# Optimization experiments

Hardware: AMD Instinct MI355X
Metric: run time of the kernel (lower is better)

## Reference

```python
import jax, jax.numpy as jnp
import numpy as np
from jax import lax

EPS = 1e-8
CAGE_SIZE = 1.4
DIST_THRESH = 0.4
CAGE_ITERS = 100
CAGE_STEP = 0.01


def _icosphere_div1():
    # icosahedron with one loop subdivision -> 42 verts, 80 faces, unit sphere
    t = (1.0 + 5.0 ** 0.5) / 2.0
    v = np.array([[-1, t, 0], [1, t, 0], [-1, -t, 0], [1, -t, 0],
                  [0, -1, t], [0, 1, t], [0, -1, -t], [0, 1, -t],
                  [t, 0, -1], [t, 0, 1], [-t, 0, -1], [-t, 0, 1]], dtype=np.float64)
    v /= np.linalg.norm(v, axis=1, keepdims=True)
    f = [[0, 11, 5], [0, 5, 1], [0, 1, 7], [0, 7, 10], [0, 10, 11],
         [1, 5, 9], [5, 11, 4], [11, 10, 2], [10, 7, 6], [7, 1, 8],
         [3, 9, 4], [3, 4, 2], [3, 2, 6], [3, 6, 8], [3, 8, 9],
         [4, 9, 5], [2, 4, 11], [6, 2, 10], [8, 6, 7], [9, 8, 1]]
    verts = list(v)
    cache = {}
    def mid(a, b):
        key = (min(a, b), max(a, b))
        if key not in cache:
            m = verts[a] + verts[b]
            verts.append(m / np.linalg.norm(m))
            cache[key] = len(verts) - 1
        return cache[key]
    nf = []
    for a, b, c in f:
        ab, bc, ca = mid(a, b), mid(b, c), mid(c, a)
        nf += [[a, ab, ca], [b, bc, ab], [c, ca, bc], [ab, bc, ca]]
    return np.stack(verts).astype(np.float32), np.array(nf, dtype=np.int32)


def _optimize_cage(cage, shape):
    # cage: (B,3,V), shape: (B,3,N). Pull cage toward origin until close to shape.
    def step(c, _):
        diff = c[:, :, :, None] - shape[:, :, None, :]          # (B,3,V,N)
        dist = jnp.sqrt(jnp.sum(diff * diff, axis=1))           # (B,V,N)
        min_d = jnp.min(dist, axis=2)                           # (B,V)
        upd = (min_d > DIST_THRESH).astype(c.dtype)
        return c + CAGE_STEP * (-c) * upd[:, None], None
    cage, _ = lax.scan(step, cage, None, length=CAGE_ITERS)
    return cage


def _mvc_weights(query, verts, faces):
    # 3D mean value coordinates (Ju et al. 2005).
    # query: (B,P,3), verts: (B,V,3), faces: (F,3) int -> weights (B,P,V)
    B, P, _ = query.shape
    V = verts.shape[1]
    F = faces.shape[0]
    u = verts[:, None] - query[:, :, None]                      # (B,P,V,3)
    d = jnp.linalg.norm(u, axis=-1)                             # (B,P,V)
    u = u / jnp.maximum(d, EPS)[..., None]
    uf = u[:, :, faces]                                         # (B,P,F,3,3)
    df = d[:, :, faces]                                         # (B,P,F,3)
    # edge lengths on unit sphere between opposite corner directions
    l = jnp.linalg.norm(jnp.roll(uf, -1, axis=3) - jnp.roll(uf, 1, axis=3), axis=-1)  # (B,P,F,3)
    theta = 2.0 * jnp.arcsin(jnp.clip(0.5 * l, 0.0, 1.0))
    h = 0.5 * jnp.sum(theta, axis=-1)                           # (B,P,F)
    sin_t = jnp.sin(theta)
    c = (2.0 * jnp.sin(h)[..., None] * jnp.sin(h[..., None] - theta)
         / jnp.maximum(jnp.roll(sin_t, -1, axis=-1) * jnp.roll(sin_t, 1, axis=-1), EPS)) - 1.0
    u0, u1, u2 = uf[..., 0, :], uf[..., 1, :], uf[..., 2, :]
    det = jnp.sum(u0 * jnp.cross(u1, u2), axis=-1)              # (B,P,F)
    s = jnp.sign(det)[..., None] * jnp.sqrt(jnp.clip(1.0 - c * c, 0.0, None))  # (B,P,F,3)
    valid = jnp.all(jnp.abs(s) > EPS, axis=-1)                  # coplanar-outside -> face contributes 0
    num = (theta - jnp.roll(c, -1, axis=-1) * jnp.roll(theta, 1, axis=-1)
           - jnp.roll(c, 1, axis=-1) * jnp.roll(theta, -1, axis=-1))
    den = df * jnp.roll(sin_t, -1, axis=-1) * jnp.roll(s, 1, axis=-1)
    den = jnp.where(jnp.abs(den) > EPS, den, jnp.where(den >= 0, EPS, -EPS))
    w = jnp.where(valid[..., None], num / den, 0.0)             # (B,P,F,3)
    W = jnp.zeros((B, P, V), dtype=query.dtype).at[:, :, faces.reshape(-1)].add(
        w.reshape(B, P, F * 3))
    sW = jnp.sum(W, axis=-1, keepdims=True)
    sW = jnp.where(jnp.abs(sW) > EPS, sW, EPS)
    return W / sW


def setup_inputs() -> dict:
    key = jax.random.key(0)
    ks = jax.random.split(key, 5)
    B, N, K = 4, 6144, 8
    v, f = _icosphere_div1()
    template_vertices = jnp.asarray(CAGE_SIZE * v.T[None])      # (1,3,42)
    return {
        "catModel": jax.random.normal(ks[0], (B, N, 3), dtype=jnp.float32),
        "catKeys": jax.random.normal(ks[1], (B, K, 3), dtype=jnp.float32),
        "catInflu": 0.1 * jax.random.normal(ks[2], (B, K, 42), dtype=jnp.float32),
        "insKeys": jax.random.normal(ks[3], (B, K, 3), dtype=jnp.float32),
        "insModel": jax.random.normal(ks[4], (B, N, 3), dtype=jnp.float32),
        "template_vertices": template_vertices,
        "template_faces": jnp.asarray(f),
    }


def reference(catModel, catKeys, catInflu, insKeys, insModel, template_vertices, template_faces):
    B = catModel.shape[0]
    cat_sh = jnp.swapaxes(catModel, 1, 2)                       # (B,3,N)
    cage = jnp.broadcast_to(template_vertices, (B,) + template_vertices.shape[1:])  # (B,3,42)
    cage = _optimize_cage(cage, cat_sh)
    # keypoint-driven cage offset via influence matrix
    kp_off = jnp.swapaxes(insKeys - catKeys, 1, 2)              # (B,3,8)
    cage_off = jnp.sum(kp_off[..., None] * catInflu[:, None], axis=2)  # (B,3,42)
    new_cage = cage + cage_off
    cage_v = jnp.swapaxes(cage, 1, 2)                           # (B,42,3)
    new_cage_v = jnp.swapaxes(new_cage, 1, 2)
    weights = _mvc_weights(catModel, cage_v, template_faces)    # (B,N,42)
    deformed = jnp.einsum('bnv,bvd->bnd', weights, new_cage_v)  # (B,N,3)
    # symmetric chamfer (squared L2, mean over points then batch, summed directions)
    d2 = jnp.sum((deformed[:, :, None] - insModel[:, None]) ** 2, axis=-1)  # (B,N,N)
    sim_loss = jnp.mean(jnp.min(d2, axis=2)) + jnp.mean(jnp.min(d2, axis=1))
    return (catModel, insModel, deformed, sim_loss)
```

## Files before the change

kernel.cpp:

```cpp
#include <hip/hip_runtime.h>
#include <hip/hip_bf16.h>
#include <math.h>

#define EPSF 1e-8f

static constexpr int FI[80][3] = {
  {0,12,14},{11,13,12},{5,14,13},{12,13,14},
  {0,14,16},{5,15,14},{1,16,15},{14,15,16},
  {0,16,18},{1,17,16},{7,18,17},{16,17,18},
  {0,18,20},{7,19,18},{10,20,19},{18,19,20},
  {0,20,12},{10,21,20},{11,12,21},{20,21,12},
  {1,15,23},{5,22,15},{9,23,22},{15,22,23},
  {5,13,25},{11,24,13},{4,25,24},{13,24,25},
  {11,21,27},{10,26,21},{2,27,26},{21,26,27},
  {10,19,29},{7,28,19},{6,29,28},{19,28,29},
  {7,17,31},{1,30,17},{8,31,30},{17,30,31},
  {3,32,34},{9,33,32},{4,34,33},{32,33,34},
  {3,34,36},{4,35,34},{2,36,35},{34,35,36},
  {3,36,38},{2,37,36},{6,38,37},{36,37,38},
  {3,38,40},{6,39,38},{8,40,39},{38,39,40},
  {3,40,32},{8,41,40},{9,32,41},{40,41,32},
  {4,33,25},{9,22,33},{5,25,22},{33,22,25},
  {2,35,27},{4,24,35},{11,27,24},{35,24,27},
  {6,37,29},{2,26,37},{10,29,26},{37,26,29},
  {8,39,31},{6,28,39},{7,31,28},{39,28,31},
  {9,41,23},{8,30,41},{1,23,30},{41,30,23}
};

__global__ __launch_bounds__(256) void k_init(unsigned* __restrict__ p, int n,
                                              float* __restrict__ loss) {
  int i = blockIdx.x * 256 + threadIdx.x;
  if (i < n) p[i] = 0x7F800000u;
  if (i == 0) loss[0] = 0.0f;
}

__global__ __launch_bounds__(512) void k_cage(
    const float* __restrict__ catModel,
    const float* __restrict__ tv,
    const float* __restrict__ catKeys,
    const float* __restrict__ insKeys,
    const float* __restrict__ catInflu,
    float* __restrict__ cage,
    float* __restrict__ ncage)
{
  const int b = blockIdx.x / 42, v = blockIdx.x % 42;
  const int tid = threadIdx.x;
  const int lane = tid & 63, w = tid >> 6;
  const float c0x = tv[v], c0y = tv[42 + v], c0z = tv[84 + v];
  const float a = c0x*c0x + c0y*c0y + c0z*c0z;

  float pb2[12], pc[12];
  const float* P = catModel + (size_t)b * 6144 * 3;
  #pragma unroll
  for (int j = 0; j < 12; ++j) {
    int n = tid + j * 512;
    float px = P[n*3+0], py = P[n*3+1], pz = P[n*3+2];
    pb2[j] = -2.0f * (c0x*px + c0y*py + c0z*pz);
    pc[j]  = px*px + py*py + pz*pz;
  }

  __shared__ int mm[8];
  __shared__ float sfin;

  int tmin = 1000;
  float s = 1.0f;
  for (int t = 0; t < 100; ++t) {
    float ma = 1e30f, mb = 1e30f, mc = 1e30f, md = 1e30f;
    #pragma unroll
    for (int j = 0; j < 12; j += 4) {
      ma = fminf(ma, fmaf(fmaf(a, s, pb2[j+0]), s, pc[j+0]));
      mb = fminf(mb, fmaf(fmaf(a, s, pb2[j+1]), s, pc[j+1]));
      mc = fminf(mc, fmaf(fmaf(a, s, pb2[j+2]), s, pc[j+2]));
      md = fminf(md, fmaf(fmaf(a, s, pb2[j+3]), s, pc[j+3]));
    }
    float m = fminf(fminf(ma, mb), fminf(mc, md));
    if (m <= 0.16f && tmin == 1000) tmin = t;
    if (__all(tmin != 1000)) break;
    s *= 0.99f;
  }

  #pragma unroll
  for (int off = 32; off; off >>= 1)
    tmin = min(tmin, __shfl_xor(tmin, off, 64));
  if (lane == 0) mm[w] = tmin;
  __syncthreads();

  if (tid == 0) {
    int k = mm[0];
    #pragma unroll
    for (int i = 1; i < 8; ++i) k = min(k, mm[i]);
    if (k > 100) k = 100;
    float sf = 1.0f;
    for (int i = 0; i < k; ++i) sf *= 0.99f;
    sfin = sf;
  }
  __syncthreads();

  if (tid < 3) {
    const int d = tid;
    const float cg = sfin * tv[d*42 + v];
    float off = 0.0f;
    #pragma unroll
    for (int k = 0; k < 8; ++k)
      off += (insKeys[(b*8+k)*3 + d] - catKeys[(b*8+k)*3 + d]) * catInflu[(b*8+k)*42 + v];
    cage [(b*42 + v)*3 + d] = cg;
    ncage[(b*42 + v)*3 + d] = cg + off;
  }
}

__global__ __launch_bounds__(256) void k_mvc(
    const float* __restrict__ catModel,
    const float* __restrict__ cage,
    const float* __restrict__ ncage,
    float* __restrict__ outCat,
    float* __restrict__ outDef)
{
  const int b    = blockIdx.x / 384;
  const int pblk = blockIdx.x % 384;
  const int lane = threadIdx.x & 63;
  const int w    = threadIdx.x >> 6;
  const int pt   = lane & 15;
  const int sub  = lane >> 4;
  const int slice = w*4 + sub;
  const int p    = pblk * 16 + pt;

  __shared__ float cv[126], nv[126];
  __shared__ unsigned sF[80];
  __shared__ float red[4][4][16];
  if (threadIdx.x < 126) {
    cv[threadIdx.x] = cage [b*126 + threadIdx.x];
    nv[threadIdx.x] = ncage[b*126 + threadIdx.x];
  }
  if (threadIdx.x < 80) {
    sF[threadIdx.x] = (unsigned)FI[threadIdx.x][0]
                    | ((unsigned)FI[threadIdx.x][1] << 8)
                    | ((unsigned)FI[threadIdx.x][2] << 16);
  }
  __syncthreads();

  const float qx = catModel[((size_t)b*6144 + p)*3 + 0];
  const float qy = catModel[((size_t)b*6144 + p)*3 + 1];
  const float qz = catModel[((size_t)b*6144 + p)*3 + 2];

  if (w == 1 && sub == 0) {
    outCat[((size_t)b*6144 + p)*3 + 0] = qx;
    outCat[((size_t)b*6144 + p)*3 + 1] = qy;
    outCat[((size_t)b*6144 + p)*3 + 2] = qz;
  }

  float sW = 0.0f, dx = 0.0f, dy = 0.0f, dz = 0.0f;

  for (int ff = 0; ff < 5; ++ff) {
    const unsigned pk = sF[slice*5 + ff];
    const int i0 = pk & 255, i1 = (pk >> 8) & 255, i2 = pk >> 16;

    float e0x = cv[i0*3+0]-qx, e0y = cv[i0*3+1]-qy, e0z = cv[i0*3+2]-qz;
    float e1x = cv[i1*3+0]-qx, e1y = cv[i1*3+1]-qy, e1z = cv[i1*3+2]-qz;
    float e2x = cv[i2*3+0]-qx, e2y = cv[i2*3+1]-qy, e2z = cv[i2*3+2]-qz;
    float d0 = sqrtf(e0x*e0x + e0y*e0y + e0z*e0z);
    float d1 = sqrtf(e1x*e1x + e1y*e1y + e1z*e1z);
    float d2 = sqrtf(e2x*e2x + e2y*e2y + e2z*e2z);
    float r0 = 1.0f / fmaxf(d0, EPSF);
    float r1 = 1.0f / fmaxf(d1, EPSF);
    float r2 = 1.0f / fmaxf(d2, EPSF);
    float u0x = e0x*r0, u0y = e0y*r0, u0z = e0z*r0;
    float u1x = e1x*r1, u1y = e1y*r1, u1z = e1z*r1;
    float u2x = e2x*r2, u2y = e2y*r2, u2z = e2z*r2;

    float ax_ = u1x-u2x, ay_ = u1y-u2y, az_ = u1z-u2z;
    float bx_ = u2x-u0x, by_ = u2y-u0y, bz_ = u2z-u0z;
    float cx_ = u0x-u1x, cy_ = u0y-u1y, cz_ = u0z-u1z;
    float l0 = sqrtf(ax_*ax_ + ay_*ay_ + az_*az_);
    float l1 = sqrtf(bx_*bx_ + by_*by_ + bz_*bz_);
    float l2 = sqrtf(cx_*cx_ + cy_*cy_ + cz_*cz_);

    float s0 = fminf(0.5f*l0, 1.0f);
    float s1 = fminf(0.5f*l1, 1.0f);
    float s2 = fminf(0.5f*l2, 1.0f);
    float th0 = 2.0f*asinf(s0), th1 = 2.0f*asinf(s1), th2 = 2.0f*asinf(s2);
    float co0 = sqrtf(fmaxf(fmaf(-s0, s0, 1.0f), 0.0f));
    float co1 = sqrtf(fmaxf(fmaf(-s1, s1, 1.0f), 0.0f));
    float co2 = sqrtf(fmaxf(fmaf(-s2, s2, 1.0f), 0.0f));
    float st0 = 2.0f*s0*co0;
    float st1 = 2.0f*s1*co1;
    float st2 = 2.0f*s2*co2;

    float Sh = s0*co1*co2 + co0*s1*co2 + co0*co1*s2 - s0*s1*s2;
    float Ch = co0*co1*co2 - s0*s1*co2 - s0*co1*s2 - co0*s1*s2;
    float sh0 = Sh*fmaf(-2.0f*s0, s0, 1.0f) - Ch*st0;
    float sh1 = Sh*fmaf(-2.0f*s1, s1, 1.0f) - Ch*st1;
    float sh2 = Sh*fmaf(-2.0f*s2, s2, 1.0f) - Ch*st2;

    float c0 = 2.0f*Sh*sh0 / fmaxf(st1*st2, EPSF) - 1.0f;
    float c1 = 2.0f*Sh*sh1 / fmaxf(st2*st0, EPSF) - 1.0f;
    float c2 = 2.0f*Sh*sh2 / fmaxf(st0*st1, EPSF) - 1.0f;

    float det = u0x*(u1y*u2z - u1z*u2y)
              + u0y*(u1z*u2x - u1x*u2z)
              + u0z*(u1x*u2y - u1y*u2x);
    float sg = (det > 0.0f) ? 1.0f : ((det < 0.0f) ? -1.0f : 0.0f);
    float q0 = sg * sqrtf(fmaxf(fmaf(-c0, c0, 1.0f), 0.0f));
    float q1 = sg * sqrtf(fmaxf(fmaf(-c1, c1, 1.0f), 0.0f));
    float q2 = sg * sqrtf(fmaxf(fmaf(-c2, c2, 1.0f), 0.0f));
    bool valid = (fabsf(q0) > EPSF) && (fabsf(q1) > EPSF) && (fabsf(q2) > EPSF);

    float n0 = th0 - c1*th2 - c2*th1;
    float n1 = th1 - c2*th0 - c0*th2;
    float n2 = th2 - c0*th1 - c1*th0;
    float de0 = d0*st1*q2;
    float de1 = d1*st2*q0;
    float de2 = d2*st0*q1;
    de0 = (fabsf(de0) > EPSF) ? de0 : ((de0 >= 0.0f) ? EPSF : -EPSF);
    de1 = (fabsf(de1) > EPSF) ? de1 : ((de1 >= 0.0f) ? EPSF : -EPSF);
    de2 = (fabsf(de2) > EPSF) ? de2 : ((de2 >= 0.0f) ? EPSF : -EPSF);

    if (valid) {
      float w0 = n0/de0, w1 = n1/de1, w2 = n2/de2;
      sW += w0 + w1 + w2;
      dx = fmaf(w0, nv[i0*3+0], fmaf(w1, nv[i1*3+0], fmaf(w2, nv[i2*3+0], dx)));
      dy = fmaf(w0, nv[i0*3+1], fmaf(w1, nv[i1*3+1], fmaf(w2, nv[i2*3+1], dy)));
      dz = fmaf(w0, nv[i0*3+2], fmaf(w1, nv[i1*3+2], fmaf(w2, nv[i2*3+2], dz)));
    }
  }

  sW += __shfl_xor(sW, 16, 64); dx += __shfl_xor(dx, 16, 64);
  dy += __shfl_xor(dy, 16, 64); dz += __shfl_xor(dz, 16, 64);
  sW += __shfl_xor(sW, 32, 64); dx += __shfl_xor(dx, 32, 64);
  dy += __shfl_xor(dy, 32, 64); dz += __shfl_xor(dz, 32, 64);

  if (sub == 0) {
    red[w][0][pt] = sW; red[w][1][pt] = dx;
    red[w][2][pt] = dy; red[w][3][pt] = dz;
  }
  __syncthreads();

  if (w == 0 && sub == 0) {
    float S = red[0][0][pt] + red[1][0][pt] + red[2][0][pt] + red[3][0][pt];
    float X = red[0][1][pt] + red[1][1][pt] + red[2][1][pt] + red[3][1][pt];
    float Y = red[0][2][pt] + red[1][2][pt] + red[2][2][pt] + red[3][2][pt];
    float Z = red[0][3][pt] + red[1][3][pt] + red[2][3][pt] + red[3][3][pt];
    S = (fabsf(S) > EPSF) ? S : EPSF;
    float inv = 1.0f / S;
    outDef[((size_t)b*6144 + p)*3 + 0] = X * inv;
    outDef[((size_t)b*6144 + p)*3 + 1] = Y * inv;
    outDef[((size_t)b*6144 + p)*3 + 2] = Z * inv;
  }
}

__global__ __launch_bounds__(256) void k_chamfer(
    const float* __restrict__ def,
    const float* __restrict__ ins,
    float*       __restrict__ outIns,
    unsigned*    __restrict__ mins)
{
  const int bx  = blockIdx.x;
  const int dir = (bx >= 384) ? 1 : 0;
  const int r   = bx - dir*384;
  const int b   = r / 96;
  const int rt  = (r % 96) / 16;
  const int cc  = r % 16;
  const int tid = threadIdx.x;

  const float* R = (dir ? ins : def) + (size_t)b * 6144 * 3;
  const float* C = (dir ? def : ins) + (size_t)b * 6144 * 3;

  const int r0 = rt*1024 + tid;
  const int r1 = r0 + 256, r2 = r0 + 512, r3 = r0 + 768;
  const float r0x = R[r0*3+0], r0y = R[r0*3+1], r0z = R[r0*3+2];
  const float r1x = R[r1*3+0], r1y = R[r1*3+1], r1z = R[r1*3+2];
  const float r2x = R[r2*3+0], r2y = R[r2*3+1], r2z = R[r2*3+2];
  const float r3x = R[r3*3+0], r3y = R[r3*3+1], r3z = R[r3*3+2];

  if (dir == 1 && cc == 0) {
    outIns[(size_t)(b*6144 + r0)*3+0] = r0x; outIns[(size_t)(b*6144 + r0)*3+1] = r0y; outIns[(size_t)(b*6144 + r0)*3+2] = r0z;
    outIns[(size_t)(b*6144 + r1)*3+0] = r1x; outIns[(size_t)(b*6144 + r1)*3+1] = r1y; outIns[(size_t)(b*6144 + r1)*3+2] = r1z;
    outIns[(size_t)(b*6144 + r2)*3+0] = r2x; outIns[(size_t)(b*6144 + r2)*3+1] = r2y; outIns[(size_t)(b*6144 + r2)*3+2] = r2z;
    outIns[(size_t)(b*6144 + r3)*3+0] = r3x; outIns[(size_t)(b*6144 + r3)*3+1] = r3y; outIns[(size_t)(b*6144 + r3)*3+2] = r3z;
  }

  __shared__ float4 tile[384];
  #pragma unroll
  for (int c = tid; c < 384; c += 256) {
    int cg = cc*384 + c;
    float cx = C[cg*3+0], cy = C[cg*3+1], cz = C[cg*3+2];
    tile[c] = make_float4(-2.0f*cx, -2.0f*cy, -2.0f*cz, cx*cx + cy*cy + cz*cz);
  }
  __syncthreads();

  float m0 = 1e30f, m1 = 1e30f, m2 = 1e30f, m3 = 1e30f;
  #pragma unroll 8
  for (int j = 0; j < 384; ++j) {
    float4 q = tile[j];
    m0 = fminf(m0, fmaf(q.x, r0x, fmaf(q.y, r0y, fmaf(q.z, r0z, q.w))));
    m1 = fminf(m1, fmaf(q.x, r1x, fmaf(q.y, r1y, fmaf(q.z, r1z, q.w))));
    m2 = fminf(m2, fmaf(q.x, r2x, fmaf(q.y, r2y, fmaf(q.z, r2z, q.w))));
    m3 = fminf(m3, fmaf(q.x, r3x, fmaf(q.y, r3y, fmaf(q.z, r3z, q.w))));
  }

  unsigned* mo = mins + dir*24576 + b*6144;
  atomicMin(&mo[r0], __float_as_uint(m0 + (r0x*r0x + r0y*r0y + r0z*r0z)));
  atomicMin(&mo[r1], __float_as_uint(m1 + (r1x*r1x + r1y*r1y + r1z*r1z)));
  atomicMin(&mo[r2], __float_as_uint(m2 + (r2x*r2x + r2y*r2y + r2z*r2z)));
  atomicMin(&mo[r3], __float_as_uint(m3 + (r3x*r3x + r3y*r3y + r3z*r3z)));
}

__global__ __launch_bounds__(256) void k_loss(
    const unsigned* __restrict__ mins,
    float* __restrict__ loss)
{
  const int base = blockIdx.x * 512 + threadIdx.x * 2;
  float s = __uint_as_float(mins[base]) + __uint_as_float(mins[base + 1]);
  #pragma unroll
  for (int off = 32; off; off >>= 1) s += __shfl_xor(s, off, 64);
  __shared__ float red[4];
  if ((threadIdx.x & 63) == 0) red[threadIdx.x >> 6] = s;
  __syncthreads();
  if (threadIdx.x == 0)
    atomicAdd(loss, (red[0] + red[1] + red[2] + red[3]) * (1.0f / 24576.0f));
}

extern "C" void kernel_launch(void* const* d_in, const int* in_sizes, int n_in,
                              void* d_out, int out_size, void* d_ws, size_t ws_size,
                              hipStream_t stream) {
  const float* catModel = (const float*)d_in[0];
  const float* catKeys  = (const float*)d_in[1];
  const float* catInflu = (const float*)d_in[2];
  const float* insKeys  = (const float*)d_in[3];
  const float* insModel = (const float*)d_in[4];
  const float* tv       = (const float*)d_in[5];

  float* out = (float*)d_out;
  float* ws  = (float*)d_ws;
  float*    cage  = ws;
  float*    ncage = ws + 512;
  unsigned* mins  = (unsigned*)(ws + 1024);

  k_init<<<192, 256, 0, stream>>>(mins, 49152, out + 221184);
  k_cage<<<168, 512, 0, stream>>>(catModel, tv, catKeys, insKeys, catInflu, cage, ncage);
  k_mvc <<<1536, 256, 0, stream>>>(catModel, cage, ncage, out, out + 147456);
  k_chamfer<<<768, 256, 0, stream>>>(out + 147456, insModel, out + 73728, mins);
  k_loss<<<96, 256, 0, stream>>>(mins, out + 221184);
}
```

Baseline: 137.6 us.

## Replace chamfer atomicMin with per-chunk partial mins and drop init kernel

The chamfer kernel now writes per-column-chunk partial minima to a workspace buffer instead of doing atomicMin into a pre-initialised array, which removes the separate init kernel launch. The loss kernel reduces across the 24 partials per row before summing. Tiling also changes from 4 rows per thread with 384-column tiles to 6 rows per thread with 256-column tiles. The cost is a larger workspace write and read (24 partials per row) and more register pressure in the chamfer kernel. The loss is zeroed by block 0 of the chamfer kernel, which relies on it running before k_loss's atomicAdd.

```diff
diff --git a/kernel.cpp b/kernel.cpp
--- a/kernel.cpp
+++ b/kernel.cpp
@@ -27,13 +27,6 @@
   {9,41,23},{8,30,41},{1,23,30},{41,30,23}
 };
 
-__global__ __launch_bounds__(256) void k_init(unsigned* __restrict__ p, int n,
-                                              float* __restrict__ loss) {
-  int i = blockIdx.x * 256 + threadIdx.x;
-  if (i < n) p[i] = 0x7F800000u;
-  if (i == 0) loss[0] = 0.0f;
-}
-
 __global__ __launch_bounds__(512) void k_cage(
     const float* __restrict__ catModel,
     const float* __restrict__ tv,
@@ -251,65 +244,83 @@
     const float* __restrict__ def,
     const float* __restrict__ ins,
     float*       __restrict__ outIns,
-    unsigned*    __restrict__ mins)
+    float*       __restrict__ partial,
+    float*       __restrict__ loss)
 {
   const int bx  = blockIdx.x;
   const int dir = (bx >= 384) ? 1 : 0;
   const int r   = bx - dir*384;
   const int b   = r / 96;
-  const int rt  = (r % 96) / 16;
-  const int cc  = r % 16;
+  const int rt  = (r % 96) / 24;
+  const int cc  = r % 24;
   const int tid = threadIdx.x;
+
+  if (bx == 0 && tid == 0) loss[0] = 0.0f;
 
   const float* R = (dir ? ins : def) + (size_t)b * 6144 * 3;
   const float* C = (dir ? def : ins) + (size_t)b * 6144 * 3;
 
-  const int r0 = rt*1024 + tid;
-  const int r1 = r0 + 256, r2 = r0 + 512, r3 = r0 + 768;
-  const float r0x = R[r0*3+0], r0y = R[r0*3+1], r0z = R[r0*3+2];
-  const float r1x = R[r1*3+0], r1y = R[r1*3+1], r1z = R[r1*3+2];
-  const float r2x = R[r2*3+0], r2y = R[r2*3+1], r2z = R[r2*3+2];
-  const float r3x = R[r3*3+0], r3y = R[r3*3+1], r3z = R[r3*3+2];
+  const int r0 = rt*1536 + tid;
+  float rx[6], ry[6], rz[6];
+  #pragma unroll
+  for (int k = 0; k < 6; ++k) {
+    int rr = r0 + k*256;
+    rx[k] = R[rr*3+0]; ry[k] = R[rr*3+1]; rz[k] = R[rr*3+2];
+  }
 
   if (dir == 1 && cc == 0) {
-    outIns[(size_t)(b*6144 + r0)*3+0] = r0x; outIns[(size_t)(b*6144 + r0)*3+1] = r0y; outIns[(size_t)(b*6144 + r0)*3+2] = r0z;
-    outIns[(size_t)(b*6144 + r1)*3+0] = r1x; outIns[(size_t)(b*6144 + r1)*3+1] = r1y; outIns[(size_t)(b*6144 + r1)*3+2] = r1z;
-    outIns[(size_t)(b*6144 + r2)*3+0] = r2x; outIns[(size_t)(b*6144 + r2)*3+1] = r2y; outIns[(size_t)(b*6144 + r2)*3+2] = r2z;
-    outIns[(size_t)(b*6144 + r3)*3+0] = r3x; outIns[(size_t)(b*6144 + r3)*3+1] = r3y; outIns[(size_t)(b*6144 + r3)*3+2] = r3z;
-  }
-
-  __shared__ float4 tile[384];
-  #pragma unroll
-  for (int c = tid; c < 384; c += 256) {
-    int cg = cc*384 + c;
-    float cx = C[cg*3+0], cy = C[cg*3+1], cz = C[cg*3+2];
-    tile[c] = make_float4(-2.0f*cx, -2.0f*cy, -2.0f*cz, cx*cx + cy*cy + cz*cz);
-  }
-  __syncthreads();
-
-  float m0 = 1e30f, m1 = 1e30f, m2 = 1e30f, m3 = 1e30f;
+    #pragma unroll
+    for (int k = 0; k < 6; ++k) {
+      int rr = r0 + k*256;
+      outIns[(size_t)(b*6144 + rr)*3+0] = rx[k];
+      outIns[(size_t)(b*6144 + rr)*3+1] = ry[k];
+      outIns[(size_t)(b*6144 + rr)*3+2] = rz[k];
+    }
+  }
+
+  __shared__ float4 tile[256];
+  {
+    int c = cc*256 + tid;
+    float cx = C[c*3+0], cy = C[c*3+1], cz = C[c*3+2];
+    tile[tid] = make_float4(-2.0f*cx, -2.0f*cy, -2.0f*cz, cx*cx + cy*cy + cz*cz);
+  }
+  __syncthreads();
+
+  float m[6];
+  #pragma unroll
+  for (int k = 0; k < 6; ++k) m[k] = 1e30f;
+
   #pragma unroll 8
-  for (int j = 0; j < 384; ++j) {
+  for (int j = 0; j < 256; ++j) {
     float4 q = tile[j];
-    m0 = fminf(m0, fmaf(q.x, r0x, fmaf(q.y, r0y, fmaf(q.z, r0z, q.w))));
-    m1 = fminf(m1, fmaf(q.x, r1x, fmaf(q.y, r1y, fmaf(q.z, r1z, q.w))));
-    m2 = fminf(m2, fmaf(q.x, r2x, fmaf(q.y, r2y, fmaf(q.z, r2z, q.w))));
-    m3 = fminf(m3, fmaf(q.x, r3x, fmaf(q.y, r3y, fmaf(q.z, r3z, q.w))));
-  }
-
-  unsigned* mo = mins + dir*24576 + b*6144;
-  atomicMin(&mo[r0], __float_as_uint(m0 + (r0x*r0x + r0y*r0y + r0z*r0z)));
-  atomicMin(&mo[r1], __float_as_uint(m1 + (r1x*r1x + r1y*r1y + r1z*r1z)));
-  atomicMin(&mo[r2], __float_as_uint(m2 + (r2x*r2x + r2y*r2y + r2z*r2z)));
-  atomicMin(&mo[r3], __float_as_uint(m3 + (r3x*r3x + r3y*r3y + r3z*r3z)));
+    #pragma unroll
+    for (int k = 0; k < 6; ++k)
+      m[k] = fminf(m[k], fmaf(q.x, rx[k], fmaf(q.y, ry[k], fmaf(q.z, rz[k], q.w))));
+  }
+
+  float* po = partial + ((size_t)((dir*4 + b)*24 + cc)) * 6144;
+  #pragma unroll
+  for (int k = 0; k < 6; ++k) {
+    int rr = r0 + k*256;
+    po[rr] = m[k] + (rx[k]*rx[k] + ry[k]*ry[k] + rz[k]*rz[k]);
+  }
 }
 
 __global__ __launch_bounds__(256) void k_loss(
-    const unsigned* __restrict__ mins,
+    const float* __restrict__ partial,
     float* __restrict__ loss)
 {
   const int base = blockIdx.x * 512 + threadIdx.x * 2;
-  float s = __uint_as_float(mins[base]) + __uint_as_float(mins[base + 1]);
+  float s = 0.0f;
+  #pragma unroll
+  for (int g = base; g < base + 2; ++g) {
+    const int db = g / 6144, row = g % 6144;
+    const float* pp = partial + (size_t)db * 24 * 6144 + row;
+    float v = 1e30f;
+    #pragma unroll
+    for (int c = 0; c < 24; ++c) v = fminf(v, pp[c * 6144]);
+    s += v;
+  }
   #pragma unroll
   for (int off = 32; off; off >>= 1) s += __shfl_xor(s, off, 64);
   __shared__ float red[4];
@@ -331,13 +342,12 @@
 
   float* out = (float*)d_out;
   float* ws  = (float*)d_ws;
-  float*    cage  = ws;
-  float*    ncage = ws + 512;
-  unsigned* mins  = (unsigned*)(ws + 1024);
-
-  k_init<<<192, 256, 0, stream>>>(mins, 49152, out + 221184);
+  float* cage    = ws;
+  float* ncage   = ws + 512;
+  float* partial = ws + 1024;
+
   k_cage<<<168, 512, 0, stream>>>(catModel, tv, catKeys, insKeys, catInflu, cage, ncage);
   k_mvc <<<1536, 256, 0, stream>>>(catModel, cage, ncage, out, out + 147456);
-  k_chamfer<<<768, 256, 0, stream>>>(out + 147456, insModel, out + 73728, mins);
-  k_loss<<<96, 256, 0, stream>>>(mins, out + 221184);
-}
+  k_chamfer<<<768, 256, 0, stream>>>(out + 147456, insModel, out + 73728, partial, out + 221184);
+  k_loss<<<96, 256, 0, stream>>>(partial, out + 221184);
+}
```

New measurement: 138.0 us. No clear change (+0.3%).
